# Kernel optimization log

Measured on AMD Instinct MI355X. Metric: run time of the kernel, lower is better.

The kernel has to match this reference:

```python
import jax, jax.numpy as jnp
import numpy as np
from functools import partial

H = 512            # LSTM_Hidden_Size
SMAX = 512         # Sentence_Max_Length
E = 300            # embedding_length


def setup_inputs() -> dict:
    key = jax.random.key(0)
    ks = jax.random.split(key, 20)
    s = 0.05
    d = {
        'inputs':  jax.random.normal(ks[0], (4096, E), jnp.float32),
        'w_ih':    jax.random.normal(ks[1], (4 * H, E), jnp.float32) * s,
        'w_hh':    jax.random.normal(ks[2], (4 * H, H), jnp.float32) * s,
        'b_ih':    jnp.zeros((4 * H,), jnp.float32),
        'b_hh':    jnp.zeros((4 * H,), jnp.float32),
        'conv1_w': jax.random.normal(ks[3], (256, 1, 7, E), jnp.float32) * s,
        'conv1_b': jnp.zeros((256,), jnp.float32),
        'conv2_w': jax.random.normal(ks[4], (64, 256, 5), jnp.float32) * s,
        'conv2_b': jnp.zeros((64,), jnp.float32),
        'conv3_w': jax.random.normal(ks[5], (256, 64, 3), jnp.float32) * s,
        'conv3_b': jnp.zeros((256,), jnp.float32),
        'conv4_w': jax.random.normal(ks[6], (16, 256, 1), jnp.float32) * s,
        'conv4_b': jnp.zeros((16,), jnp.float32),
        'fc1_w':   jax.random.normal(ks[7], (128, H + 16 * (SMAX // 8)), jnp.float32) * s,
        'fc1_b':   jnp.zeros((128,), jnp.float32),
        'fc2_w':   jax.random.normal(ks[8], (32, 128), jnp.float32) * s,
        'fc2_b':   jnp.zeros((32,), jnp.float32),
        'fc3_w':   jax.random.normal(ks[9], (1, 32), jnp.float32) * s,
        'fc3_b':   jnp.zeros((1,), jnp.float32),
    }
    return d


def _maxpool1d_2(x):  # x: [N, C, L] -> [N, C, L//2]
    return jax.lax.reduce_window(x, -jnp.inf, jax.lax.max,
                                 (1, 1, 2), (1, 1, 2), 'VALID')


def _conv1d(x, w, b, pad):  # x: [N,C,L], w: [O,I,K]
    y = jax.lax.conv_general_dilated(x, w, (1,), [(pad, pad)],
                                     dimension_numbers=('NCH', 'OIH', 'NCH'))
    return y + b[None, :, None]


def _forward(inputs, w_ih, w_hh, b_ih, b_hh,
             conv1_w, conv1_b, conv2_w, conv2_b, conv3_w, conv3_b,
             conv4_w, conv4_b, fc1_w, fc1_b, fc2_w, fc2_b, fc3_w, fc3_b):
    T = inputs.shape[0]
    sig, tanh = jax.nn.sigmoid, jnp.tanh

    # --- LSTMCell scan over time (batch = 1, state kept as [H]) ---
    def step(carry, x_t):
        h, c = carry
        gates = x_t @ w_ih.T + b_ih + h @ w_hh.T + b_hh  # [4H]
        i, f, g, o = jnp.split(gates, 4)
        c_new = sig(f) * c + sig(i) * tanh(g)
        h_new = sig(o) * tanh(c_new)
        return (h_new, c_new), h_new

    init = (jnp.zeros((H,), inputs.dtype), jnp.zeros((H,), inputs.dtype))
    _, hxs = jax.lax.scan(step, init, inputs)      # [T, H]
    hx_mean = jnp.mean(hxs, axis=0, keepdims=True)  # [1, H]

    # --- CNN branch on first SMAX rows, zero-padded if T < SMAX ---
    L = min(SMAX, T)
    x0 = jnp.zeros((1, 1, SMAX, E), inputs.dtype).at[:, :, :L, :].set(inputs[:L][None, None])
    y = jax.lax.conv_general_dilated(x0, conv1_w, (1, 1), [(3, 3), (0, 0)],
                                     dimension_numbers=('NCHW', 'OIHW', 'NCHW'))
    y = (y + conv1_b[None, :, None, None]).squeeze(3)   # [1, 256, SMAX]
    y = sig(_maxpool1d_2(y))                            # [1, 256, SMAX/2]
    y = sig(_maxpool1d_2(_conv1d(y, conv2_w, conv2_b, 2)))  # [1, 64, SMAX/4]
    y = sig(_maxpool1d_2(_conv1d(y, conv3_w, conv3_b, 1)))  # [1, 256, SMAX/8]
    y = sig(_conv1d(y, conv4_w, conv4_b, 0))                 # [1, 16, SMAX/8]
    y = y.reshape(1, -1)                                     # [1, 1024]

    # --- MLP head ---
    x = jnp.concatenate([hx_mean, y], axis=1)  # [1, 1536]
    x = sig(x @ fc1_w.T + fc1_b)
    x = sig(x @ fc2_w.T + fc2_b)
    x = sig(x @ fc3_w.T + fc3_b)
    return x


def reference(inputs, w_ih, w_hh, b_ih, b_hh,
              conv1_w, conv1_b, conv2_w, conv2_b, conv3_w, conv3_b,
              conv4_w, conv4_b, fc1_w, fc1_b, fc2_w, fc2_b, fc3_w, fc3_b):
    return _forward(inputs, w_ih, w_hh, b_ih, b_hh,
                    conv1_w, conv1_b, conv2_w, conv2_b, conv3_w, conv3_b,
                    conv4_w, conv4_b, fc1_w, fc1_b, fc2_w, fc2_b, fc3_w, fc3_b)
```

## Files before the change

kernel.cpp:

```cpp
#include <hip/hip_runtime.h>
#include <hip/hip_bf16.h>


#define HSZ   512
#define ESZ   300
#define NBLK  64

typedef unsigned long long u64t;
typedef float f32x4 __attribute__((ext_vector_type(4)));
typedef unsigned u32x4 __attribute__((ext_vector_type(4)));

__device__ __forceinline__ float sigf(float x) {
    return 1.f / (1.f + __expf(-x));
}
__device__ __forceinline__ float tanh_fast(float x) {
    return 1.f - 2.f / (__expf(2.f * x) + 1.f);
}

__device__ __forceinline__ f32x4 ldg_f4(const f32x4* p) {
    f32x4 v;
    asm volatile("global_load_dwordx4 %0, %1, off\n\ts_waitcnt vmcnt(0)"
                 : "=v"(v) : "v"(p));
    return v;
}
__device__ __forceinline__ u32x4 ld_x4_coh(const void* p) {
    u32x4 v;
    asm volatile("global_load_dwordx4 %0, %1, off sc0 sc1\n\ts_waitcnt vmcnt(0)"
                 : "=v"(v) : "v"(p) : "memory");
    return v;
}
#define AGLD64(p)   __hip_atomic_load((p), __ATOMIC_RELAXED, __HIP_MEMORY_SCOPE_AGENT)

__global__ __attribute__((amdgpu_flat_work_group_size(256, 256),
                          amdgpu_waves_per_eu(1, 1)))
void lstm_fast(
    const float* __restrict__ G, const float* __restrict__ w_hh,
    u64t* hpack , float* hmean , int T)
{
    __shared__ float hlds[2][512];
    const int tid  = threadIdx.x;
    const int lane = tid & 63;
    const int wave = tid >> 6;
    const int dot  = tid >> 3;
    const int seg  = tid & 7;
    const int gate = dot & 3;
    const int jl   = dot >> 2;
    const int j    = blockIdx.x * 8 + jl;
    const int row  = gate * HSZ + j;

    f32x4 wh[16];
    {
        const f32x4* whp = (const f32x4*)(w_hh + (size_t)row * HSZ);
#pragma unroll
        for (int i = 0; i < 16; ++i)
            wh[i] = ldg_f4(whp + (seg * 16 + ((i + seg) & 15)));
    }

    float c = 0.f, hsum = 0.f;
    const int l0 = lane & 32;
    const int j2 = blockIdx.x * 8 + wave * 2 + (lane >> 5);

    for (int s = 1; s <= T; ++s) {
        const int t = s - 1, p = t & 1;

        float acc = (seg == 0) ? G[(size_t)t * (4 * HSZ) + row] : 0.f;

        {
            const u32x4* pp = (const u32x4*)(hpack + (size_t)p * HSZ) + tid;
            const unsigned tg = (unsigned)t;
            u32x4 v = ld_x4_coh(pp);
            while (v[1] != tg || v[3] != tg)
                v = ld_x4_coh(pp);
            hlds[p][2 * tid]     = __uint_as_float(v[0]);
            hlds[p][2 * tid + 1] = __uint_as_float(v[2]);
        }
        __syncthreads();

        {
            const f32x4* hp = (const f32x4*)(&hlds[p][0]);
#pragma unroll
            for (int i = 0; i < 16; ++i) {
                f32x4 h4 = hp[seg * 16 + ((i + seg) & 15)];
                acc += wh[i][0] * h4[0] + wh[i][1] * h4[1] +
                       wh[i][2] * h4[2] + wh[i][3] * h4[3];
            }
        }
        acc += __shfl_xor(acc, 4, 64);
        acc += __shfl_xor(acc, 2, 64);
        acc += __shfl_xor(acc, 1, 64);
        float gi = __shfl(acc, l0 + 0,  64);
        float gf = __shfl(acc, l0 + 8,  64);
        float gg = __shfl(acc, l0 + 16, 64);
        float go = __shfl(acc, l0 + 24, 64);

        float is = sigf(gi), fs = sigf(gf), os = sigf(go);
        float gt = tanh_fast(gg);
        c = fs * c + is * gt;
        float h = os * tanh_fast(c);

        if ((lane & 31) == 0) {
            hsum += h;
            union { float f; unsigned u; } hv; hv.f = h;
            u64t pk = ((u64t)(unsigned)s << 32) | (u64t)hv.u;
            u64t old = __hip_atomic_exchange(
                &hpack[(size_t)(s & 1) * HSZ + j2], pk,
                __ATOMIC_RELAXED, __HIP_MEMORY_SCOPE_AGENT);
            asm volatile("" :: "v"(old));
        }
    }

    if ((lane & 31) == 0)
        hmean[j2] = hsum * (1.f / (float)T);
}

__global__ __launch_bounds__(256, 1) void lstm_small(
    const float* __restrict__ inputs, const float* __restrict__ w_ih,
    const float* __restrict__ w_hh, const float* __restrict__ b_ih,
    const float* __restrict__ b_hh,
    u64t* hpack, float* hmean, int T)
{
    __shared__ float hlds[2][512];
    const int tid  = threadIdx.x;
    const int lane = tid & 63;
    const int wave = tid >> 6;
    const int dot  = tid >> 3;
    const int seg  = tid & 7;
    const int gate = dot & 3;
    const int jl   = dot >> 2;
    const int j    = blockIdx.x * 8 + jl;
    const int row  = gate * HSZ + j;

    f32x4 wh[16]; int offs[16];
    const f32x4* whp = (const f32x4*)(w_hh + (size_t)row * HSZ);
#pragma unroll
    for (int i = 0; i < 16; ++i) {
        int cc = seg * 16 + ((i + seg) & 15);
        offs[i] = cc;
        wh[i] = ldg_f4(whp + cc);
    }
    const int base = (seg == 7) ? 260 : seg * 40;
    float wx[40];
#pragma unroll
    for (int i = 0; i < 40; ++i) {
        bool valid = (seg < 7) || (i >= 20);
        wx[i] = valid ? w_ih[(size_t)row * ESZ + base + i] : 0.f;
    }
    const float bias = b_ih[row] + b_hh[row];

    float c = 0.f, hsum = 0.f;
    const int l0 = lane & 32;
    const int j2 = blockIdx.x * 8 + wave * 2 + (lane >> 5);

    for (int s = 1; s <= T; ++s) {
        const int t = s - 1, p = t & 1;
        float acc = (seg == 0) ? bias : 0.f;
        const float4* xp4 = (const float4*)(inputs + (size_t)t * ESZ + base);
#pragma unroll
        for (int i4 = 0; i4 < 10; ++i4) {
            float4 x4 = xp4[i4];
            acc += wx[i4*4+0]*x4.x + wx[i4*4+1]*x4.y +
                   wx[i4*4+2]*x4.z + wx[i4*4+3]*x4.w;
        }
        {
            u64t* w0p = hpack + (size_t)p * HSZ + tid;
            u64t* w1p = w0p + 256;
            const unsigned tg = (unsigned)t;
            u64t v0 = AGLD64(w0p), v1 = AGLD64(w1p);
            bool r0 = false, r1 = false;
            while (true) {
                r0 = r0 || ((unsigned)(v0 >> 32) == tg);
                r1 = r1 || ((unsigned)(v1 >> 32) == tg);
                if (r0 && r1) break;
                u64t n0 = AGLD64(w0p), n1 = AGLD64(w1p);
                if (!r0) v0 = n0;
                if (!r1) v1 = n1;
            }
            hlds[p][tid]       = __uint_as_float((unsigned)v0);
            hlds[p][tid + 256] = __uint_as_float((unsigned)v1);
        }
        __syncthreads();
        const f32x4* hp = (const f32x4*)(&hlds[p][0]);
#pragma unroll
        for (int i = 0; i < 16; ++i) {
            f32x4 h4 = hp[offs[i]];
            acc += wh[i][0]*h4[0] + wh[i][1]*h4[1] + wh[i][2]*h4[2] + wh[i][3]*h4[3];
        }
        acc += __shfl_xor(acc, 4, 64);
        acc += __shfl_xor(acc, 2, 64);
        acc += __shfl_xor(acc, 1, 64);
        float gi = __shfl(acc, l0 + 0,  64);
        float gf = __shfl(acc, l0 + 8,  64);
        float gg = __shfl(acc, l0 + 16, 64);
        float go = __shfl(acc, l0 + 24, 64);
        float is = sigf(gi), fs = sigf(gf), os = sigf(go);
        float gt = tanh_fast(gg);
        c = fs * c + is * gt;
        float h = os * tanh_fast(c);
        if ((lane & 31) == 0) {
            union { float f; unsigned u; } hv; hv.f = h;
            __hip_atomic_store(&hpack[(size_t)(s & 1) * HSZ + j2],
                               ((u64t)(unsigned)s << 32) | (u64t)hv.u,
                               __ATOMIC_RELAXED, __HIP_MEMORY_SCOPE_AGENT);
            hsum += h;
        }
    }
    if ((lane & 31) == 0) hmean[j2] = hsum * (1.f / (float)T);
}

__global__ __launch_bounds__(256) void gemm_g(
    const float* __restrict__ A, const float* __restrict__ B,
    const float* __restrict__ bi, const float* __restrict__ bh,
    float* __restrict__ C, int M, int N, int K)
{
    __shared__ float As[16][65];
    __shared__ float Bs[16][65];
    const int tid = threadIdx.x;
    const int m0 = blockIdx.y * 64, n0 = blockIdx.x * 64;
    const int tm = (tid >> 4) * 4, tn = (tid & 15) * 4;
    const int lr = tid >> 2;
    const int lk = (tid & 3) * 4;
    float acc[4][4] = {};

    for (int kk = 0; kk < K; kk += 16) {
        int k0 = kk + lk;
        float4 av = {0,0,0,0}, bv = {0,0,0,0};
        if (m0 + lr < M) {
            const float* ap = A + (size_t)(m0 + lr) * K;
            if (k0 + 3 < K) av = *(const float4*)(ap + k0);
            else {
                float tmp[4];
#pragma unroll
                for (int e = 0; e < 4; ++e) tmp[e] = (k0 + e < K) ? ap[k0 + e] : 0.f;
                av.x = tmp[0]; av.y = tmp[1]; av.z = tmp[2]; av.w = tmp[3];
            }
        }
        {
            const float* bp = B + (size_t)(n0 + lr) * K;
            if (k0 + 3 < K) bv = *(const float4*)(bp + k0);
            else {
                float tmp[4];
#pragma unroll
                for (int e = 0; e < 4; ++e) tmp[e] = (k0 + e < K) ? bp[k0 + e] : 0.f;
                bv.x = tmp[0]; bv.y = tmp[1]; bv.z = tmp[2]; bv.w = tmp[3];
            }
        }
        As[lk+0][lr] = av.x; As[lk+1][lr] = av.y;
        As[lk+2][lr] = av.z; As[lk+3][lr] = av.w;
        Bs[lk+0][lr] = bv.x; Bs[lk+1][lr] = bv.y;
        Bs[lk+2][lr] = bv.z; Bs[lk+3][lr] = bv.w;
        __syncthreads();
#pragma unroll
        for (int k2 = 0; k2 < 16; ++k2) {
            float a0 = As[k2][tm], a1 = As[k2][tm+1], a2 = As[k2][tm+2], a3 = As[k2][tm+3];
            float b0 = Bs[k2][tn], b1 = Bs[k2][tn+1], b2 = Bs[k2][tn+2], b3 = Bs[k2][tn+3];
            acc[0][0]+=a0*b0; acc[0][1]+=a0*b1; acc[0][2]+=a0*b2; acc[0][3]+=a0*b3;
            acc[1][0]+=a1*b0; acc[1][1]+=a1*b1; acc[1][2]+=a1*b2; acc[1][3]+=a1*b3;
            acc[2][0]+=a2*b0; acc[2][1]+=a2*b1; acc[2][2]+=a2*b2; acc[2][3]+=a2*b3;
            acc[3][0]+=a3*b0; acc[3][1]+=a3*b1; acc[3][2]+=a3*b2; acc[3][3]+=a3*b3;
        }
        __syncthreads();
    }
#pragma unroll
    for (int i = 0; i < 4; ++i) {
        int m = m0 + tm + i;
        if (m >= M) break;
#pragma unroll
        for (int jj = 0; jj < 4; ++jj) {
            int n = n0 + tn + jj;
            C[(size_t)m * N + n] = acc[i][jj] + bi[n] + bh[n];
        }
    }
}

__global__ __launch_bounds__(256) void gemm32(
    const float* __restrict__ A, const float* __restrict__ B,
    const float* __restrict__ bias, float* __restrict__ C,
    int M, int N, int K)
{
    __shared__ float As[32][33];
    __shared__ float Bs[32][33];
    const int tid = threadIdx.x;
    const int m0 = blockIdx.y * 32, n0 = blockIdx.x * 32;
    const int tn = (tid & 15) * 2, tm = (tid >> 4) * 2;
    float a00 = 0, a01 = 0, a10 = 0, a11 = 0;

    for (int kk = 0; kk < K; kk += 32) {
        const int k = tid & 31, r = tid >> 5;
#pragma unroll
        for (int jj = 0; jj < 4; ++jj) {
            int m = r + jj * 8;
            As[k][m] = (kk + k < K && m0 + m < M) ? A[(size_t)(m0+m)*K + kk+k] : 0.f;
            Bs[k][m] = (kk + k < K && n0 + m < N) ? B[(size_t)(n0+m)*K + kk+k] : 0.f;
        }
        __syncthreads();
#pragma unroll
        for (int k2 = 0; k2 < 32; ++k2) {
            float x0 = As[k2][tm], x1 = As[k2][tm+1];
            float y0 = Bs[k2][tn], y1 = Bs[k2][tn+1];
            a00 += x0*y0; a01 += x0*y1; a10 += x1*y0; a11 += x1*y1;
        }
        __syncthreads();
    }
    const int m = m0 + tm, n = n0 + tn;
    if (m < M) {
        if (n     < N) C[(size_t)m*N + n]     = a00 + bias[n];
        if (n + 1 < N) C[(size_t)m*N + n + 1] = a01 + bias[n+1];
    }
    if (m + 1 < M) {
        if (n     < N) C[(size_t)(m+1)*N + n]     = a10 + bias[n];
        if (n + 1 < N) C[(size_t)(m+1)*N + n + 1] = a11 + bias[n+1];
    }
}

__global__ void im2col1(const float* __restrict__ in, float* __restrict__ X)
{
    int idx = blockIdx.x * 256 + threadIdx.x;
    if (idx >= 512 * 2100) return;
    int t = idx / 2100, k = idx - t * 2100;
    int dt = k / 300, e = k - dt * 300;
    int tt = t + dt - 3;
    X[idx] = (tt >= 0 && tt < 512) ? in[tt * 300 + e] : 0.f;
}

__global__ void im2colN(const float* __restrict__ S, float* __restrict__ X,
                        int L, int Cin, int KW, int pad, int total)
{
    int idx = blockIdx.x * 256 + threadIdx.x;
    if (idx >= total) return;
    int KC = Cin * KW;
    int t = idx / KC, r = idx - t * KC;
    int c = r / KW, dk = r - c * KW;
    int tt = t + dk - pad;
    X[idx] = (tt >= 0 && tt < L) ? S[c * L + tt] : 0.f;
}

__global__ void transpose4(const float* __restrict__ S, float* __restrict__ X)
{
    int idx = blockIdx.x * 256 + threadIdx.x;
    if (idx >= 64 * 256) return;
    int t = idx >> 8, c = idx & 255;
    X[idx] = S[c * 64 + t];
}

__global__ void poolsig(const float* __restrict__ Cin_, float* __restrict__ S,
                        int Cch, int LP)
{
    int idx = blockIdx.x * 256 + threadIdx.x;
    if (idx >= Cch * LP) return;
    int c = idx / LP, tp = idx - c * LP;
    float a = Cin_[(2 * tp) * Cch + c];
    float b = Cin_[(2 * tp + 1) * Cch + c];
    S[idx] = sigf(fmaxf(a, b));
}

__global__ void sigy(const float* __restrict__ C4, float* __restrict__ y)
{
    int idx = blockIdx.x * 256 + threadIdx.x;
    if (idx >= 1024) return;
    int o = idx >> 6, t = idx & 63;
    y[idx] = sigf(C4[t * 16 + o]);
}

__global__ void fc1_kernel(const float* __restrict__ hmean,
                           const float* __restrict__ y,
                           const float* __restrict__ w,
                           const float* __restrict__ b,
                           float* __restrict__ out)
{
    int k = blockIdx.x, lane = threadIdx.x;
    float a = 0.f;
    for (int i = lane; i < 1536; i += 64) {
        float xv = (i < 512) ? hmean[i] : y[i - 512];
        a += xv * w[k * 1536 + i];
    }
#pragma unroll
    for (int off = 32; off; off >>= 1) a += __shfl_xor(a, off, 64);
    if (lane == 0) out[k] = sigf(a + b[k]);
}

__global__ void head_kernel(const float* __restrict__ x2,
                            const float* __restrict__ w2, const float* __restrict__ b2,
                            const float* __restrict__ w3, const float* __restrict__ b3,
                            float* __restrict__ out)
{
    __shared__ float x3[32];
    int lane = threadIdx.x;
    if (lane < 32) {
        float a = 0.f;
        for (int i = 0; i < 128; ++i) a += x2[i] * w2[lane * 128 + i];
        x3[lane] = sigf(a + b2[lane]);
    }
    __syncthreads();
    if (lane == 0) {
        float a = 0.f;
        for (int i = 0; i < 32; ++i) a += x3[i] * w3[i];
        out[0] = sigf(a + b3[0]);
    }
}

extern "C" void kernel_launch(void* const* d_in, const int* in_sizes, int n_in,
                              void* d_out, int out_size, void* d_ws, size_t ws_size,
                              hipStream_t stream)
{
    const float* inputs = (const float*)d_in[0];
    const float* w_ih   = (const float*)d_in[1];
    const float* w_hh   = (const float*)d_in[2];
    const float* b_ih   = (const float*)d_in[3];
    const float* b_hh   = (const float*)d_in[4];
    const float* c1w    = (const float*)d_in[5];
    const float* c1b    = (const float*)d_in[6];
    const float* c2w    = (const float*)d_in[7];
    const float* c2b    = (const float*)d_in[8];
    const float* c3w    = (const float*)d_in[9];
    const float* c3b    = (const float*)d_in[10];
    const float* c4w    = (const float*)d_in[11];
    const float* c4b    = (const float*)d_in[12];
    const float* fc1w   = (const float*)d_in[13];
    const float* fc1b   = (const float*)d_in[14];
    const float* fc2w   = (const float*)d_in[15];
    const float* fc2b   = (const float*)d_in[16];
    const float* fc3w   = (const float*)d_in[17];
    const float* fc3b   = (const float*)d_in[18];
    float* out = (float*)d_out;
    const int T = in_sizes[0] / ESZ;

    float*    p     = (float*)d_ws;
    u64t*     hpack = (u64t*)d_ws;
    float* hmean = p + 2048;
    float* X1 = p + 2560;
    float* C1 = X1 + 1075200;
    float* s1 = C1 + 131072;
    float* X2 = s1 + 65536;
    float* C2 = X2 + 327680;
    float* s2 = C2 + 16384;
    float* X3 = s2 + 8192;
    float* C3 = X3 + 24576;
    float* s3 = C3 + 32768;
    float* X4 = s3 + 16384;
    float* C4 = X4 + 16384;
    float* yb = C4 + 1024;
    float* x2 = yb + 1024;
    float* G  = x2 + 128;
    const size_t need_bytes = ((size_t)(x2 + 128 - p) + (size_t)T * 2048) * 4;
    const bool use_g = ws_size >= need_bytes;

    hipMemsetAsync(d_ws, 0, 8192, stream);

    if (use_g) {
        gemm_g<<<dim3(2048 / 64, (T + 63) / 64), 256, 0, stream>>>(
            inputs, w_ih, b_ih, b_hh, G, T, 2048, ESZ);
        lstm_fast<<<NBLK, 256, 0, stream>>>(G, w_hh, hpack, hmean, T);
    } else {
        lstm_small<<<NBLK, 256, 0, stream>>>(
            inputs, w_ih, w_hh, b_ih, b_hh, hpack, hmean, T);
    }

    im2col1<<<4200, 256, 0, stream>>>(inputs, X1);
    gemm32<<<dim3(8, 16), 256, 0, stream>>>(X1, c1w, c1b, C1, 512, 256, 2100);
    poolsig<<<256, 256, 0, stream>>>(C1, s1, 256, 256);

    im2colN<<<1280, 256, 0, stream>>>(s1, X2, 256, 256, 5, 2, 256 * 1280);
    gemm32<<<dim3(2, 8), 256, 0, stream>>>(X2, c2w, c2b, C2, 256, 64, 1280);
    poolsig<<<32, 256, 0, stream>>>(C2, s2, 64, 128);

    im2colN<<<96, 256, 0, stream>>>(s2, X3, 128, 64, 3, 1, 128 * 192);
    gemm32<<<dim3(8, 4), 256, 0, stream>>>(X3, c3w, c3b, C3, 128, 256, 192);
    poolsig<<<64, 256, 0, stream>>>(C3, s3, 256, 64);

    transpose4<<<64, 256, 0, stream>>>(s3, X4);
    gemm32<<<dim3(1, 2), 256, 0, stream>>>(X4, c4w, c4b, C4, 64, 16, 256);
    sigy<<<4, 256, 0, stream>>>(C4, yb);

    fc1_kernel<<<128, 64, 0, stream>>>(hmean, yb, fc1w, fc1b, x2);
    head_kernel<<<1, 64, 0, stream>>>(x2, fc2w, fc2b, fc3w, fc3b, out);
}
```

Measured before the change: 7.033 ms.

## Pack step tag into low mantissa bits and poll with staggered in-flight loads

The cross-block hidden-state exchange now stores each h value as a 32-bit word: the mantissa is rounded so its low 8 bits are free, and those bits carry the step tag. Before, each value was a 64-bit (value, step) pair. The poll loop is hand-written assembly that keeps three pairs of coherent loads in flight, with short sleeps between them, so a fresh value is seen sooner and the polling latency of the serial LSTM recurrence is cut. In exchange, h loses 8 bits of mantissa precision, and the tag wraps at 256 steps, which relies on the two-buffer lockstep scheme.

```diff
diff --git a/kernel.cpp b/kernel.cpp
--- a/kernel.cpp
+++ b/kernel.cpp
@@ -8,7 +8,6 @@
 
 typedef unsigned long long u64t;
 typedef float f32x4 __attribute__((ext_vector_type(4)));
-typedef unsigned u32x4 __attribute__((ext_vector_type(4)));
 
 __device__ __forceinline__ float sigf(float x) {
     return 1.f / (1.f + __expf(-x));
@@ -23,19 +22,13 @@
                  : "=v"(v) : "v"(p));
     return v;
 }
-__device__ __forceinline__ u32x4 ld_x4_coh(const void* p) {
-    u32x4 v;
-    asm volatile("global_load_dwordx4 %0, %1, off sc0 sc1\n\ts_waitcnt vmcnt(0)"
-                 : "=v"(v) : "v"(p) : "memory");
-    return v;
-}
 #define AGLD64(p)   __hip_atomic_load((p), __ATOMIC_RELAXED, __HIP_MEMORY_SCOPE_AGENT)
 
 __global__ __attribute__((amdgpu_flat_work_group_size(256, 256),
                           amdgpu_waves_per_eu(1, 1)))
 void lstm_fast(
     const float* __restrict__ G, const float* __restrict__ w_hh,
-    u64t* hpack , float* hmean , int T)
+    unsigned* hp32 , float* hmean , int T)
 {
     __shared__ float hlds[2][512];
     const int tid  = threadIdx.x;
@@ -60,19 +53,74 @@
     const int l0 = lane & 32;
     const int j2 = blockIdx.x * 8 + wave * 2 + (lane >> 5);
 
+    unsigned w0a = 0, w1a = 0, w0b = 0, w1b = 0, w0c = 0, w1c = 0;
+
     for (int s = 1; s <= T; ++s) {
         const int t = s - 1, p = t & 1;
 
         float acc = (seg == 0) ? G[(size_t)t * (4 * HSZ) + row] : 0.f;
 
         {
-            const u32x4* pp = (const u32x4*)(hpack + (size_t)p * HSZ) + tid;
-            const unsigned tg = (unsigned)t;
-            u32x4 v = ld_x4_coh(pp);
-            while (v[1] != tg || v[3] != tg)
-                v = ld_x4_coh(pp);
-            hlds[p][2 * tid]     = __uint_as_float(v[0]);
-            hlds[p][2 * tid + 1] = __uint_as_float(v[2]);
+            unsigned* ap = hp32 + (size_t)p * HSZ + 2 * tid;
+            const unsigned tg = (unsigned)t & 255u;
+            unsigned h0u, h1u, tmp;
+            asm volatile(
+                "global_load_dword %[w0a], %[ad], off sc0 sc1\n\t"
+                "global_load_dword %[w1a], %[ad], off offset:4 sc0 sc1\n\t"
+                "s_sleep 5\n\t"
+                "global_load_dword %[w0b], %[ad], off sc0 sc1\n\t"
+                "global_load_dword %[w1b], %[ad], off offset:4 sc0 sc1\n\t"
+                "s_sleep 5\n\t"
+                "global_load_dword %[w0c], %[ad], off sc0 sc1\n\t"
+                "global_load_dword %[w1c], %[ad], off offset:4 sc0 sc1\n\t"
+                "Lpoll_%=:\n\t"
+                "s_waitcnt vmcnt(4)\n\t"
+                "v_xor_b32 %[tmp], %[w0a], %[tg]\n\t"
+                "v_xor_b32 %[h1], %[w1a], %[tg]\n\t"
+                "v_or_b32 %[tmp], %[tmp], %[h1]\n\t"
+                "v_and_b32 %[tmp], 255, %[tmp]\n\t"
+                "v_cmp_ne_u32 vcc, 0, %[tmp]\n\t"
+                "s_cbranch_vccz Lgota_%=\n\t"
+                "global_load_dword %[w0a], %[ad], off sc0 sc1\n\t"
+                "global_load_dword %[w1a], %[ad], off offset:4 sc0 sc1\n\t"
+                "s_waitcnt vmcnt(4)\n\t"
+                "v_xor_b32 %[tmp], %[w0b], %[tg]\n\t"
+                "v_xor_b32 %[h1], %[w1b], %[tg]\n\t"
+                "v_or_b32 %[tmp], %[tmp], %[h1]\n\t"
+                "v_and_b32 %[tmp], 255, %[tmp]\n\t"
+                "v_cmp_ne_u32 vcc, 0, %[tmp]\n\t"
+                "s_cbranch_vccz Lgotb_%=\n\t"
+                "global_load_dword %[w0b], %[ad], off sc0 sc1\n\t"
+                "global_load_dword %[w1b], %[ad], off offset:4 sc0 sc1\n\t"
+                "s_waitcnt vmcnt(4)\n\t"
+                "v_xor_b32 %[tmp], %[w0c], %[tg]\n\t"
+                "v_xor_b32 %[h1], %[w1c], %[tg]\n\t"
+                "v_or_b32 %[tmp], %[tmp], %[h1]\n\t"
+                "v_and_b32 %[tmp], 255, %[tmp]\n\t"
+                "v_cmp_ne_u32 vcc, 0, %[tmp]\n\t"
+                "s_cbranch_vccz Lgotc_%=\n\t"
+                "global_load_dword %[w0c], %[ad], off sc0 sc1\n\t"
+                "global_load_dword %[w1c], %[ad], off offset:4 sc0 sc1\n\t"
+                "s_branch Lpoll_%=\n\t"
+                "Lgota_%=:\n\t"
+                "v_mov_b32 %[h0], %[w0a]\n\t"
+                "v_mov_b32 %[h1], %[w1a]\n\t"
+                "s_branch Lend_%=\n\t"
+                "Lgotb_%=:\n\t"
+                "v_mov_b32 %[h0], %[w0b]\n\t"
+                "v_mov_b32 %[h1], %[w1b]\n\t"
+                "s_branch Lend_%=\n\t"
+                "Lgotc_%=:\n\t"
+                "v_mov_b32 %[h0], %[w0c]\n\t"
+                "v_mov_b32 %[h1], %[w1c]\n\t"
+                "Lend_%=:"
+                : [h0]"=&v"(h0u), [h1]"=&v"(h1u), [tmp]"=&v"(tmp),
+                  [w0a]"+v"(w0a), [w1a]"+v"(w1a), [w0b]"+v"(w0b),
+                  [w1b]"+v"(w1b), [w0c]"+v"(w0c), [w1c]"+v"(w1c)
+                : [ad]"v"(ap), [tg]"v"(tg)
+                : "vcc", "memory");
+            hlds[p][2 * tid]     = __uint_as_float(h0u & ~255u);
+            hlds[p][2 * tid + 1] = __uint_as_float(h1u & ~255u);
         }
         __syncthreads();
 
@@ -99,13 +147,13 @@
         float h = os * tanh_fast(c);
 
         if ((lane & 31) == 0) {
-            hsum += h;
-            union { float f; unsigned u; } hv; hv.f = h;
-            u64t pk = ((u64t)(unsigned)s << 32) | (u64t)hv.u;
-            u64t old = __hip_atomic_exchange(
-                &hpack[(size_t)(s & 1) * HSZ + j2], pk,
+            unsigned hb = ((__float_as_uint(h) + 128u) & ~255u) |
+                          ((unsigned)s & 255u);
+            unsigned old = __hip_atomic_exchange(
+                &hp32[(size_t)(s & 1) * HSZ + j2], hb,
                 __ATOMIC_RELAXED, __HIP_MEMORY_SCOPE_AGENT);
             asm volatile("" :: "v"(old));
+            hsum += h;
         }
     }
 
@@ -425,6 +473,7 @@
     const int T = in_sizes[0] / ESZ;
 
     float*    p     = (float*)d_ws;
+    unsigned* hp32  = (unsigned*)d_ws;
     u64t*     hpack = (u64t*)d_ws;
     float* hmean = p + 2048;
     float* X1 = p + 2560;
@@ -449,7 +498,7 @@
     if (use_g) {
         gemm_g<<<dim3(2048 / 64, (T + 63) / 64), 256, 0, stream>>>(
             inputs, w_ih, b_ih, b_hh, G, T, 2048, ESZ);
-        lstm_fast<<<NBLK, 256, 0, stream>>>(G, w_hh, hpack, hmean, T);
+        lstm_fast<<<NBLK, 256, 0, stream>>>(G, w_hh, hp32, hmean, T);
     } else {
         lstm_small<<<NBLK, 256, 0, stream>>>(
             inputs, w_ih, w_hh, b_ih, b_hh, hpack, hmean, T);
```

After: 7.207 ms. 1.02x slower.

## Fuse whole forward into one persistent kernel overlapping LSTM with input GEMM and CNN

Applied to the files above, without the earlier changes.

Replaces the chain of separate launches with a single 256-block persistent kernel. 64 blocks run the LSTM recurrence and wait on per-row-tile counters, so they can start as soon as the first 64-timestep slice of the input projection G is ready instead of waiting for the whole GEMM. The other 192 blocks compute the G tiles, then the CNN branch with software grid barriers between stages, and finally the MLP head after the LSTM blocks signal completion. This removes launch overhead and serialization between the LSTM and CNN branches. It depends on all 256 blocks being co-resident, since the spin barriers would deadlock otherwise, and the CNN stages now share only 192 blocks.

```diff
diff --git a/kernel.cpp b/kernel.cpp
--- a/kernel.cpp
+++ b/kernel.cpp
@@ -2,9 +2,10 @@
 #include <hip/hip_bf16.h>
 
 
-#define HSZ   512
-#define ESZ   300
-#define NBLK  64
+#define HSZ    512
+#define ESZ    300
+#define NBLK   64
+#define NBCNN  192
 
 typedef unsigned long long u64t;
 typedef float f32x4 __attribute__((ext_vector_type(4)));
@@ -29,88 +30,365 @@
                  : "=v"(v) : "v"(p) : "memory");
     return v;
 }
-#define AGLD64(p)   __hip_atomic_load((p), __ATOMIC_RELAXED, __HIP_MEMORY_SCOPE_AGENT)
+#define AGLD64(p) __hip_atomic_load((p), __ATOMIC_RELAXED, __HIP_MEMORY_SCOPE_AGENT)
+
+__device__ __forceinline__ void rel_add(int* p) {
+    __hip_atomic_fetch_add(p, 1, __ATOMIC_RELEASE, __HIP_MEMORY_SCOPE_AGENT);
+}
+__device__ __forceinline__ int rlx_ld(const int* p) {
+    return __hip_atomic_load(p, __ATOMIC_RELAXED, __HIP_MEMORY_SCOPE_AGENT);
+}
+__device__ __forceinline__ int acq_ld(const int* p) {
+    return __hip_atomic_load(p, __ATOMIC_ACQUIRE, __HIP_MEMORY_SCOPE_AGENT);
+}
+
+__device__ __forceinline__ void cnn_barrier(int* cnt, int expected) {
+    __syncthreads();
+    if (threadIdx.x == 0) {
+        rel_add(cnt);
+        while (rlx_ld(cnt) < expected) __builtin_amdgcn_s_sleep(2);
+        (void)acq_ld(cnt);
+    }
+    __syncthreads();
+}
+
+__device__ void gemm_g_tile(const float* __restrict__ A, const float* __restrict__ B,
+                            const float* __restrict__ bi, const float* __restrict__ bh,
+                            float* __restrict__ C, int M, int N, int K,
+                            int m0, int n0, float (&As)[16][65], float (&Bs)[16][65])
+{
+    const int tid = threadIdx.x;
+    const int tm = (tid >> 4) * 4, tn = (tid & 15) * 4;
+    const int lr = tid >> 2;
+    const int lk = (tid & 3) * 4;
+    float acc[4][4] = {};
+
+    for (int kk = 0; kk < K; kk += 16) {
+        int k0 = kk + lk;
+        float4 av = {0,0,0,0}, bv = {0,0,0,0};
+        if (m0 + lr < M) {
+            const float* ap = A + (size_t)(m0 + lr) * K;
+            if (k0 + 3 < K) av = *(const float4*)(ap + k0);
+            else {
+                float tmp[4];
+#pragma unroll
+                for (int e = 0; e < 4; ++e) tmp[e] = (k0 + e < K) ? ap[k0 + e] : 0.f;
+                av.x = tmp[0]; av.y = tmp[1]; av.z = tmp[2]; av.w = tmp[3];
+            }
+        }
+        {
+            const float* bp = B + (size_t)(n0 + lr) * K;
+            if (k0 + 3 < K) bv = *(const float4*)(bp + k0);
+            else {
+                float tmp[4];
+#pragma unroll
+                for (int e = 0; e < 4; ++e) tmp[e] = (k0 + e < K) ? bp[k0 + e] : 0.f;
+                bv.x = tmp[0]; bv.y = tmp[1]; bv.z = tmp[2]; bv.w = tmp[3];
+            }
+        }
+        As[lk+0][lr] = av.x; As[lk+1][lr] = av.y;
+        As[lk+2][lr] = av.z; As[lk+3][lr] = av.w;
+        Bs[lk+0][lr] = bv.x; Bs[lk+1][lr] = bv.y;
+        Bs[lk+2][lr] = bv.z; Bs[lk+3][lr] = bv.w;
+        __syncthreads();
+#pragma unroll
+        for (int k2 = 0; k2 < 16; ++k2) {
+            float a0 = As[k2][tm], a1 = As[k2][tm+1], a2 = As[k2][tm+2], a3 = As[k2][tm+3];
+            float b0 = Bs[k2][tn], b1 = Bs[k2][tn+1], b2 = Bs[k2][tn+2], b3 = Bs[k2][tn+3];
+            acc[0][0]+=a0*b0; acc[0][1]+=a0*b1; acc[0][2]+=a0*b2; acc[0][3]+=a0*b3;
+            acc[1][0]+=a1*b0; acc[1][1]+=a1*b1; acc[1][2]+=a1*b2; acc[1][3]+=a1*b3;
+            acc[2][0]+=a2*b0; acc[2][1]+=a2*b1; acc[2][2]+=a2*b2; acc[2][3]+=a2*b3;
+            acc[3][0]+=a3*b0; acc[3][1]+=a3*b1; acc[3][2]+=a3*b2; acc[3][3]+=a3*b3;
+        }
+        __syncthreads();
+    }
+#pragma unroll
+    for (int i = 0; i < 4; ++i) {
+        int m = m0 + tm + i;
+        if (m >= M) break;
+#pragma unroll
+        for (int jj = 0; jj < 4; ++jj) {
+            int n = n0 + tn + jj;
+            C[(size_t)m * N + n] = acc[i][jj] + bi[n] + bh[n];
+        }
+    }
+}
+
+__device__ void gemm32_tile(const float* __restrict__ A, const float* __restrict__ B,
+                            const float* __restrict__ bias, float* __restrict__ C,
+                            int M, int N, int K, int m0, int n0,
+                            float (&As)[32][33], float (&Bs)[32][33])
+{
+    const int tid = threadIdx.x;
+    const int tn = (tid & 15) * 2, tm = (tid >> 4) * 2;
+    float a00 = 0, a01 = 0, a10 = 0, a11 = 0;
+
+    for (int kk = 0; kk < K; kk += 32) {
+        const int k = tid & 31, r = tid >> 5;
+#pragma unroll
+        for (int jj = 0; jj < 4; ++jj) {
+            int m = r + jj * 8;
+            As[k][m] = (kk + k < K && m0 + m < M) ? A[(size_t)(m0+m)*K + kk+k] : 0.f;
+            Bs[k][m] = (kk + k < K && n0 + m < N) ? B[(size_t)(n0+m)*K + kk+k] : 0.f;
+        }
+        __syncthreads();
+#pragma unroll
+        for (int k2 = 0; k2 < 32; ++k2) {
+            float x0 = As[k2][tm], x1 = As[k2][tm+1];
+            float y0 = Bs[k2][tn], y1 = Bs[k2][tn+1];
+            a00 += x0*y0; a01 += x0*y1; a10 += x1*y0; a11 += x1*y1;
+        }
+        __syncthreads();
+    }
+    const int m = m0 + tm, n = n0 + tn;
+    if (m < M) {
+        if (n     < N) C[(size_t)m*N + n]     = a00 + bias[n];
+        if (n + 1 < N) C[(size_t)m*N + n + 1] = a01 + bias[n+1];
+    }
+    if (m + 1 < M) {
+        if (n     < N) C[(size_t)(m+1)*N + n]     = a10 + bias[n];
+        if (n + 1 < N) C[(size_t)(m+1)*N + n + 1] = a11 + bias[n+1];
+    }
+}
 
 __global__ __attribute__((amdgpu_flat_work_group_size(256, 256),
                           amdgpu_waves_per_eu(1, 1)))
-void lstm_fast(
-    const float* __restrict__ G, const float* __restrict__ w_hh,
-    u64t* hpack , float* hmean , int T)
+void mega_kernel(
+    const float* __restrict__ inputs, const float* __restrict__ w_ih,
+    const float* __restrict__ w_hh, const float* __restrict__ b_ih,
+    const float* __restrict__ b_hh,
+    const float* __restrict__ c1w, const float* __restrict__ c1b,
+    const float* __restrict__ c2w, const float* __restrict__ c2b,
+    const float* __restrict__ c3w, const float* __restrict__ c3b,
+    const float* __restrict__ c4w, const float* __restrict__ c4b,
+    const float* __restrict__ fc1w, const float* __restrict__ fc1b,
+    const float* __restrict__ fc2w, const float* __restrict__ fc2b,
+    const float* __restrict__ fc3w, const float* __restrict__ fc3b,
+    float* __restrict__ out,
+    u64t* hpack, float* hmean, int* gtile_cnt, int* stage_cnt, int* lstm_done,
+    float* G, float* X1, float* C1, float* s1, float* X2, float* C2,
+    float* s2, float* X3, float* C3, float* s3, float* X4, float* C4,
+    float* yb, float* x2buf, int T)
 {
     __shared__ float hlds[2][512];
-    const int tid  = threadIdx.x;
-    const int lane = tid & 63;
-    const int wave = tid >> 6;
-    const int dot  = tid >> 3;
-    const int seg  = tid & 7;
-    const int gate = dot & 3;
-    const int jl   = dot >> 2;
-    const int j    = blockIdx.x * 8 + jl;
-    const int row  = gate * HSZ + j;
-
-    f32x4 wh[16];
+    __shared__ float AsG[16][65];
+    __shared__ float BsG[16][65];
+    __shared__ float As[32][33];
+    __shared__ float Bs[32][33];
+    __shared__ float xhead[32];
+
+    const int tid = threadIdx.x;
+    const int bid = blockIdx.x;
+
+    if (bid < NBLK) {
+        const int lane = tid & 63;
+        const int wave = tid >> 6;
+        const int dot  = tid >> 3;
+        const int seg  = tid & 7;
+        const int gate = dot & 3;
+        const int jl   = dot >> 2;
+        const int j    = bid * 8 + jl;
+        const int row  = gate * HSZ + j;
+
+        f32x4 wh[16];
+        {
+            const f32x4* whp = (const f32x4*)(w_hh + (size_t)row * HSZ);
+#pragma unroll
+            for (int i = 0; i < 16; ++i)
+                wh[i] = ldg_f4(whp + (seg * 16 + ((i + seg) & 15)));
+        }
+
+        float c = 0.f, hsum = 0.f;
+        const int l0 = lane & 32;
+        const int j2 = bid * 8 + wave * 2 + (lane >> 5);
+
+        for (int s = 1; s <= T; ++s) {
+            const int t = s - 1, p = t & 1;
+
+            if ((t & 63) == 0) {
+                if (tid == 0) {
+                    int* gc = &gtile_cnt[t >> 6];
+                    while (rlx_ld(gc) < 32) __builtin_amdgcn_s_sleep(1);
+                    (void)acq_ld(gc);
+                }
+                __syncthreads();
+            }
+
+            float acc = (seg == 0) ? G[(size_t)t * (4 * HSZ) + row] : 0.f;
+
+            {
+                const u32x4* pp = (const u32x4*)(hpack + (size_t)p * HSZ) + tid;
+                const unsigned tg = (unsigned)t;
+                u32x4 v = ld_x4_coh(pp);
+                while (v[1] != tg || v[3] != tg)
+                    v = ld_x4_coh(pp);
+                hlds[p][2 * tid]     = __uint_as_float(v[0]);
+                hlds[p][2 * tid + 1] = __uint_as_float(v[2]);
+            }
+            __syncthreads();
+
+            {
+                const f32x4* hp = (const f32x4*)(&hlds[p][0]);
+#pragma unroll
+                for (int i = 0; i < 16; ++i) {
+                    f32x4 h4 = hp[seg * 16 + ((i + seg) & 15)];
+                    acc += wh[i][0] * h4[0] + wh[i][1] * h4[1] +
+                           wh[i][2] * h4[2] + wh[i][3] * h4[3];
+                }
+            }
+            acc += __shfl_xor(acc, 4, 64);
+            acc += __shfl_xor(acc, 2, 64);
+            acc += __shfl_xor(acc, 1, 64);
+            float gi = __shfl(acc, l0 + 0,  64);
+            float gf = __shfl(acc, l0 + 8,  64);
+            float gg = __shfl(acc, l0 + 16, 64);
+            float go = __shfl(acc, l0 + 24, 64);
+
+            float is = sigf(gi), fs = sigf(gf), os = sigf(go);
+            float gt = tanh_fast(gg);
+            c = fs * c + is * gt;
+            float h = os * tanh_fast(c);
+
+            if ((lane & 31) == 0) {
+                hsum += h;
+                union { float f; unsigned u; } hv; hv.f = h;
+                u64t pk = ((u64t)(unsigned)s << 32) | (u64t)hv.u;
+                u64t old = __hip_atomic_exchange(
+                    &hpack[(size_t)(s & 1) * HSZ + j2], pk,
+                    __ATOMIC_RELAXED, __HIP_MEMORY_SCOPE_AGENT);
+                asm volatile("" :: "v"(old));
+            }
+        }
+
+        if ((lane & 31) == 0)
+            hmean[j2] = hsum * (1.f / (float)T);
+        __syncthreads();
+        if (tid == 0) rel_add(lstm_done);
+        return;
+    }
+
+    const int cb = bid - NBLK;
+    int exp = NBCNN;
+
     {
-        const f32x4* whp = (const f32x4*)(w_hh + (size_t)row * HSZ);
-#pragma unroll
-        for (int i = 0; i < 16; ++i)
-            wh[i] = ldg_f4(whp + (seg * 16 + ((i + seg) & 15)));
-    }
-
-    float c = 0.f, hsum = 0.f;
-    const int l0 = lane & 32;
-    const int j2 = blockIdx.x * 8 + wave * 2 + (lane >> 5);
-
-    for (int s = 1; s <= T; ++s) {
-        const int t = s - 1, p = t & 1;
-
-        float acc = (seg == 0) ? G[(size_t)t * (4 * HSZ) + row] : 0.f;
-
-        {
-            const u32x4* pp = (const u32x4*)(hpack + (size_t)p * HSZ) + tid;
-            const unsigned tg = (unsigned)t;
-            u32x4 v = ld_x4_coh(pp);
-            while (v[1] != tg || v[3] != tg)
-                v = ld_x4_coh(pp);
-            hlds[p][2 * tid]     = __uint_as_float(v[0]);
-            hlds[p][2 * tid + 1] = __uint_as_float(v[2]);
+        const int n_mt = (T + 63) >> 6;
+        const int total = n_mt * 32;
+        for (int tile = cb; tile < total; tile += NBCNN) {
+            const int mt = tile >> 5, nt = tile & 31;
+            gemm_g_tile(inputs, w_ih, b_ih, b_hh, G, T, 2048, ESZ,
+                        mt * 64, nt * 64, AsG, BsG);
+            __syncthreads();
+            if (tid == 0) rel_add(&gtile_cnt[mt]);
+        }
+    }
+
+    for (int idx = cb * 256 + tid; idx < 512 * 2100; idx += NBCNN * 256) {
+        int t_ = idx / 2100, k = idx - t_ * 2100;
+        int dt = k / 300, e = k - dt * 300;
+        int tt = t_ + dt - 3;
+        X1[idx] = (tt >= 0 && tt < 512) ? inputs[tt * 300 + e] : 0.f;
+    }
+    cnn_barrier(stage_cnt, exp); exp += NBCNN;
+
+    for (int tile = cb; tile < 128; tile += NBCNN)
+        gemm32_tile(X1, c1w, c1b, C1, 512, 256, 2100,
+                    (tile >> 3) * 32, (tile & 7) * 32, As, Bs);
+    cnn_barrier(stage_cnt, exp); exp += NBCNN;
+
+    for (int idx = cb * 256 + tid; idx < 256 * 256; idx += NBCNN * 256) {
+        int c_ = idx >> 8, tp = idx & 255;
+        float a = C1[(2 * tp) * 256 + c_], b = C1[(2 * tp + 1) * 256 + c_];
+        s1[idx] = sigf(fmaxf(a, b));
+    }
+    cnn_barrier(stage_cnt, exp); exp += NBCNN;
+
+    for (int idx = cb * 256 + tid; idx < 256 * 1280; idx += NBCNN * 256) {
+        int t_ = idx / 1280, r = idx - t_ * 1280;
+        int c_ = r / 5, dk = r - c_ * 5;
+        int tt = t_ + dk - 2;
+        X2[idx] = (tt >= 0 && tt < 256) ? s1[c_ * 256 + tt] : 0.f;
+    }
+    cnn_barrier(stage_cnt, exp); exp += NBCNN;
+
+    for (int tile = cb; tile < 16; tile += NBCNN)
+        gemm32_tile(X2, c2w, c2b, C2, 256, 64, 1280,
+                    (tile >> 1) * 32, (tile & 1) * 32, As, Bs);
+    cnn_barrier(stage_cnt, exp); exp += NBCNN;
+
+    for (int idx = cb * 256 + tid; idx < 64 * 128; idx += NBCNN * 256) {
+        int c_ = idx / 128, tp = idx - c_ * 128;
+        float a = C2[(2 * tp) * 64 + c_], b = C2[(2 * tp + 1) * 64 + c_];
+        s2[idx] = sigf(fmaxf(a, b));
+    }
+    cnn_barrier(stage_cnt, exp); exp += NBCNN;
+
+    for (int idx = cb * 256 + tid; idx < 128 * 192; idx += NBCNN * 256) {
+        int t_ = idx / 192, r = idx - t_ * 192;
+        int c_ = r / 3, dk = r - c_ * 3;
+        int tt = t_ + dk - 1;
+        X3[idx] = (tt >= 0 && tt < 128) ? s2[c_ * 128 + tt] : 0.f;
+    }
+    cnn_barrier(stage_cnt, exp); exp += NBCNN;
+
+    for (int tile = cb; tile < 32; tile += NBCNN)
+        gemm32_tile(X3, c3w, c3b, C3, 128, 256, 192,
+                    (tile >> 3) * 32, (tile & 7) * 32, As, Bs);
+    cnn_barrier(stage_cnt, exp); exp += NBCNN;
+
+    for (int idx = cb * 256 + tid; idx < 256 * 64; idx += NBCNN * 256) {
+        int c_ = idx / 64, tp = idx - c_ * 64;
+        float a = C3[(2 * tp) * 256 + c_], b = C3[(2 * tp + 1) * 256 + c_];
+        s3[idx] = sigf(fmaxf(a, b));
+    }
+    cnn_barrier(stage_cnt, exp); exp += NBCNN;
+
+    for (int idx = cb * 256 + tid; idx < 64 * 256; idx += NBCNN * 256) {
+        int t_ = idx >> 8, c_ = idx & 255;
+        X4[idx] = s3[c_ * 64 + t_];
+    }
+    cnn_barrier(stage_cnt, exp); exp += NBCNN;
+
+    for (int tile = cb; tile < 2; tile += NBCNN)
+        gemm32_tile(X4, c4w, c4b, C4, 64, 16, 256, tile * 32, 0, As, Bs);
+    cnn_barrier(stage_cnt, exp); exp += NBCNN;
+
+    for (int idx = cb * 256 + tid; idx < 1024; idx += NBCNN * 256) {
+        int o = idx >> 6, t_ = idx & 63;
+        yb[idx] = sigf(C4[t_ * 16 + o]);
+    }
+    cnn_barrier(stage_cnt, exp); exp += NBCNN;
+
+    if (tid == 0) {
+        while (rlx_ld(lstm_done) < NBLK) __builtin_amdgcn_s_sleep(8);
+        (void)acq_ld(lstm_done);
+    }
+    __syncthreads();
+
+    if (cb < 128 && tid < 64) {
+        float a = 0.f;
+        for (int i = tid; i < 1536; i += 64) {
+            float xv = (i < 512) ? hmean[i] : yb[i - 512];
+            a += xv * fc1w[cb * 1536 + i];
+        }
+#pragma unroll
+        for (int off = 32; off; off >>= 1) a += __shfl_xor(a, off, 64);
+        if (tid == 0) x2buf[cb] = sigf(a + fc1b[cb]);
+    }
+    cnn_barrier(stage_cnt, exp); exp += NBCNN;
+
+    if (cb == 0) {
+        if (tid < 32) {
+            float a = 0.f;
+            for (int i = 0; i < 128; ++i) a += x2buf[i] * fc2w[tid * 128 + i];
+            xhead[tid] = sigf(a + fc2b[tid]);
         }
         __syncthreads();
-
-        {
-            const f32x4* hp = (const f32x4*)(&hlds[p][0]);
-#pragma unroll
-            for (int i = 0; i < 16; ++i) {
-                f32x4 h4 = hp[seg * 16 + ((i + seg) & 15)];
-                acc += wh[i][0] * h4[0] + wh[i][1] * h4[1] +
-                       wh[i][2] * h4[2] + wh[i][3] * h4[3];
-            }
-        }
-        acc += __shfl_xor(acc, 4, 64);
-        acc += __shfl_xor(acc, 2, 64);
-        acc += __shfl_xor(acc, 1, 64);
-        float gi = __shfl(acc, l0 + 0,  64);
-        float gf = __shfl(acc, l0 + 8,  64);
-        float gg = __shfl(acc, l0 + 16, 64);
-        float go = __shfl(acc, l0 + 24, 64);
-
-        float is = sigf(gi), fs = sigf(gf), os = sigf(go);
-        float gt = tanh_fast(gg);
-        c = fs * c + is * gt;
-        float h = os * tanh_fast(c);
-
-        if ((lane & 31) == 0) {
-            hsum += h;
-            union { float f; unsigned u; } hv; hv.f = h;
-            u64t pk = ((u64t)(unsigned)s << 32) | (u64t)hv.u;
-            u64t old = __hip_atomic_exchange(
-                &hpack[(size_t)(s & 1) * HSZ + j2], pk,
-                __ATOMIC_RELAXED, __HIP_MEMORY_SCOPE_AGENT);
-            asm volatile("" :: "v"(old));
-        }
-    }
-
-    if ((lane & 31) == 0)
-        hmean[j2] = hsum * (1.f / (float)T);
+        if (tid == 0) {
+            float a = 0.f;
+            for (int i = 0; i < 32; ++i) a += xhead[i] * fc3w[i];
+            out[0] = sigf(a + fc3b[0]);
+        }
+    }
 }
 
 __global__ __launch_bounds__(256, 1) void lstm_small(
@@ -207,71 +485,6 @@
     if ((lane & 31) == 0) hmean[j2] = hsum * (1.f / (float)T);
 }
 
-__global__ __launch_bounds__(256) void gemm_g(
-    const float* __restrict__ A, const float* __restrict__ B,
-    const float* __restrict__ bi, const float* __restrict__ bh,
-    float* __restrict__ C, int M, int N, int K)
-{
-    __shared__ float As[16][65];
-    __shared__ float Bs[16][65];
-    const int tid = threadIdx.x;
-    const int m0 = blockIdx.y * 64, n0 = blockIdx.x * 64;
-    const int tm = (tid >> 4) * 4, tn = (tid & 15) * 4;
-    const int lr = tid >> 2;
-    const int lk = (tid & 3) * 4;
-    float acc[4][4] = {};
-
-    for (int kk = 0; kk < K; kk += 16) {
-        int k0 = kk + lk;
-        float4 av = {0,0,0,0}, bv = {0,0,0,0};
-        if (m0 + lr < M) {
-            const float* ap = A + (size_t)(m0 + lr) * K;
-            if (k0 + 3 < K) av = *(const float4*)(ap + k0);
-            else {
-                float tmp[4];
-#pragma unroll
-                for (int e = 0; e < 4; ++e) tmp[e] = (k0 + e < K) ? ap[k0 + e] : 0.f;
-                av.x = tmp[0]; av.y = tmp[1]; av.z = tmp[2]; av.w = tmp[3];
-            }
-        }
-        {
-            const float* bp = B + (size_t)(n0 + lr) * K;
-            if (k0 + 3 < K) bv = *(const float4*)(bp + k0);
-            else {
-                float tmp[4];
-#pragma unroll
-                for (int e = 0; e < 4; ++e) tmp[e] = (k0 + e < K) ? bp[k0 + e] : 0.f;
-                bv.x = tmp[0]; bv.y = tmp[1]; bv.z = tmp[2]; bv.w = tmp[3];
-            }
-        }
-        As[lk+0][lr] = av.x; As[lk+1][lr] = av.y;
-        As[lk+2][lr] = av.z; As[lk+3][lr] = av.w;
-        Bs[lk+0][lr] = bv.x; Bs[lk+1][lr] = bv.y;
-        Bs[lk+2][lr] = bv.z; Bs[lk+3][lr] = bv.w;
-        __syncthreads();
-#pragma unroll
-        for (int k2 = 0; k2 < 16; ++k2) {
-            float a0 = As[k2][tm], a1 = As[k2][tm+1], a2 = As[k2][tm+2], a3 = As[k2][tm+3];
-            float b0 = Bs[k2][tn], b1 = Bs[k2][tn+1], b2 = Bs[k2][tn+2], b3 = Bs[k2][tn+3];
-            acc[0][0]+=a0*b0; acc[0][1]+=a0*b1; acc[0][2]+=a0*b2; acc[0][3]+=a0*b3;
-            acc[1][0]+=a1*b0; acc[1][1]+=a1*b1; acc[1][2]+=a1*b2; acc[1][3]+=a1*b3;
-            acc[2][0]+=a2*b0; acc[2][1]+=a2*b1; acc[2][2]+=a2*b2; acc[2][3]+=a2*b3;
-            acc[3][0]+=a3*b0; acc[3][1]+=a3*b1; acc[3][2]+=a3*b2; acc[3][3]+=a3*b3;
-        }
-        __syncthreads();
-    }
-#pragma unroll
-    for (int i = 0; i < 4; ++i) {
-        int m = m0 + tm + i;
-        if (m >= M) break;
-#pragma unroll
-        for (int jj = 0; jj < 4; ++jj) {
-            int n = n0 + tn + jj;
-            C[(size_t)m * N + n] = acc[i][jj] + bi[n] + bh[n];
-        }
-    }
-}
-
 __global__ __launch_bounds__(256) void gemm32(
     const float* __restrict__ A, const float* __restrict__ B,
     const float* __restrict__ bias, float* __restrict__ C,
@@ -279,37 +492,7 @@
 {
     __shared__ float As[32][33];
     __shared__ float Bs[32][33];
-    const int tid = threadIdx.x;
-    const int m0 = blockIdx.y * 32, n0 = blockIdx.x * 32;
-    const int tn = (tid & 15) * 2, tm = (tid >> 4) * 2;
-    float a00 = 0, a01 = 0, a10 = 0, a11 = 0;
-
-    for (int kk = 0; kk < K; kk += 32) {
-        const int k = tid & 31, r = tid >> 5;
-#pragma unroll
-        for (int jj = 0; jj < 4; ++jj) {
-            int m = r + jj * 8;
-            As[k][m] = (kk + k < K && m0 + m < M) ? A[(size_t)(m0+m)*K + kk+k] : 0.f;
-            Bs[k][m] = (kk + k < K && n0 + m < N) ? B[(size_t)(n0+m)*K + kk+k] : 0.f;
-        }
-        __syncthreads();
-#pragma unroll
-        for (int k2 = 0; k2 < 32; ++k2) {
-            float x0 = As[k2][tm], x1 = As[k2][tm+1];
-            float y0 = Bs[k2][tn], y1 = Bs[k2][tn+1];
-            a00 += x0*y0; a01 += x0*y1; a10 += x1*y0; a11 += x1*y1;
-        }
-        __syncthreads();
-    }
-    const int m = m0 + tm, n = n0 + tn;
-    if (m < M) {
-        if (n     < N) C[(size_t)m*N + n]     = a00 + bias[n];
-        if (n + 1 < N) C[(size_t)m*N + n + 1] = a01 + bias[n+1];
-    }
-    if (m + 1 < M) {
-        if (n     < N) C[(size_t)(m+1)*N + n]     = a10 + bias[n];
-        if (n + 1 < N) C[(size_t)(m+1)*N + n + 1] = a11 + bias[n+1];
-    }
+    gemm32_tile(A, B, bias, C, M, N, K, blockIdx.y * 32, blockIdx.x * 32, As, Bs);
 }
 
 __global__ void im2col1(const float* __restrict__ in, float* __restrict__ X)
@@ -424,10 +607,13 @@
     float* out = (float*)d_out;
     const int T = in_sizes[0] / ESZ;
 
-    float*    p     = (float*)d_ws;
-    u64t*     hpack = (u64t*)d_ws;
-    float* hmean = p + 2048;
-    float* X1 = p + 2560;
+    float* p         = (float*)d_ws;
+    u64t*  hpack     = (u64t*)d_ws;
+    int*   gtile_cnt = (int*)d_ws + 2048;
+    int*   stage_cnt = (int*)d_ws + 2176;
+    int*   lstm_done = (int*)d_ws + 2177;
+    float* hmean = p + 2560;
+    float* X1 = p + 3072;
     float* C1 = X1 + 1075200;
     float* s1 = C1 + 131072;
     float* X2 = s1 + 65536;
@@ -444,16 +630,20 @@
     const size_t need_bytes = ((size_t)(x2 + 128 - p) + (size_t)T * 2048) * 4;
     const bool use_g = ws_size >= need_bytes;
 
-    hipMemsetAsync(d_ws, 0, 8192, stream);
+    hipMemsetAsync(d_ws, 0, 10240, stream);
 
     if (use_g) {
-        gemm_g<<<dim3(2048 / 64, (T + 63) / 64), 256, 0, stream>>>(
-            inputs, w_ih, b_ih, b_hh, G, T, 2048, ESZ);
-        lstm_fast<<<NBLK, 256, 0, stream>>>(G, w_hh, hpack, hmean, T);
-    } else {
-        lstm_small<<<NBLK, 256, 0, stream>>>(
-            inputs, w_ih, w_hh, b_ih, b_hh, hpack, hmean, T);
-    }
+        mega_kernel<<<256, 256, 0, stream>>>(
+            inputs, w_ih, w_hh, b_ih, b_hh,
+            c1w, c1b, c2w, c2b, c3w, c3b, c4w, c4b,
+            fc1w, fc1b, fc2w, fc2b, fc3w, fc3b, out,
+            hpack, hmean, gtile_cnt, stage_cnt, lstm_done,
+            G, X1, C1, s1, X2, C2, s2, X3, C3, s3, X4, C4, yb, x2, T);
+        return;
+    }
+
+    lstm_small<<<NBLK, 256, 0, stream>>>(
+        inputs, w_ih, w_hh, b_ih, b_hh, hpack, hmean, T);
 
     im2col1<<<4200, 256, 0, stream>>>(inputs, X1);
     gemm32<<<dim3(8, 16), 256, 0, stream>>>(X1, c1w, c1b, C1, 512, 256, 2100);
```

Result: faster. 6.707 ms (-4.6%).
